# Kernel optimization log

Measured on AMD Instinct MI355X. Metric: run time of the kernel, lower is better.

## Reference

```python
import jax, jax.numpy as jnp
import numpy as np

LN_EPS = 1e-5


def entmax15(z):
    # exact 1.5-entmax over last axis (Peters & Martins sorting algorithm)
    z = z / 2.0
    z = z - jnp.max(z, axis=-1, keepdims=True)  # shift-invariant, for stability
    zs = -jnp.sort(-z, axis=-1)                 # descending sort
    k = jnp.arange(1, z.shape[-1] + 1, dtype=z.dtype)
    mean = jnp.cumsum(zs, axis=-1) / k
    meansq = jnp.cumsum(zs * zs, axis=-1) / k
    ss = k * (meansq - jnp.square(mean))
    delta = (1.0 - ss) / k
    tau = mean - jnp.sqrt(jnp.clip(delta, 0.0))
    support = jnp.sum((tau <= zs).astype(jnp.int32), axis=-1, keepdims=True)
    tau_star = jnp.take_along_axis(tau, support - 1, axis=-1)
    return jnp.square(jnp.clip(z - tau_star, 0.0))


def layernorm_noaffine(v):
    m = jnp.mean(v, axis=-1, keepdims=True)
    var = jnp.mean(jnp.square(v - m), axis=-1, keepdims=True)
    return (v - m) / jnp.sqrt(var + LN_EPS)


def cp_mumoe(x, gate, Win, Wout):
    ones = jnp.ones(x.shape[:-1] + (1,), x.dtype)
    xb = jnp.concatenate([x, ones], axis=-1)
    z = jnp.einsum('btd,dr->btr', xb, Win) * gate  # [b,t,R]
    return jnp.einsum('btr,or->bto', z, Wout)      # [b,t,o]


def setup_inputs() -> dict:
    key = jax.random.key(0)
    ks = jax.random.split(key, 8)
    B, T, D, O, D2, E, R = 8, 2048, 1024, 4096, 1024, 16, 512
    s = lambda k, shape, scale: jax.random.normal(k, shape, jnp.float32) * scale
    return {
        'x': s(ks[0], (B, T, D), 1.0),
        'proj': s(ks[1], (D, E), D ** -0.5),
        'C1': s(ks[2], (E, R), E ** -0.5),
        'Win1': s(ks[3], (D + 1, R), D ** -0.5),
        'Wout1': s(ks[4], (O, R), R ** -0.5),
        'C2': s(ks[5], (E, R), E ** -0.5),
        'Win2': s(ks[6], (O + 1, R), O ** -0.5),
        'Wout2': s(ks[7], (D2, R), R ** -0.5),
    }


def reference(x, proj, C1, Win1, Wout1, C2, Win2, Wout2):
    # expert gating: projection -> LN (no affine) -> 1.5-entmax
    a = entmax15(layernorm_noaffine(jnp.einsum('btd,de->bte', x, proj)))  # [b,t,E]
    # layer 1: CP-decomposed expert mixture (bias folded into input mode)
    g1 = jnp.einsum('bte,er->btr', a, C1)
    h = cp_mumoe(x, g1, Win1, Wout1)
    # GELU + layer 2 reusing the same gate coefficients
    h = jax.nn.gelu(h, approximate=False)
    g2 = jnp.einsum('bte,er->btr', a, C2)
    return cp_mumoe(h, g2, Win2, Wout2)
```

## Files before the change

kernel.cpp:

```cpp
#include <hip/hip_runtime.h>
#include <hip/hip_bf16.h>
#include <math.h>
#include <stdint.h>

typedef unsigned short u16;
typedef __attribute__((ext_vector_type(8))) short bf16x8;
typedef __attribute__((ext_vector_type(4))) float f32x4;
typedef __attribute__((address_space(3))) void* as3_void;
typedef const __attribute__((address_space(1))) void* as1_cvoid;

__device__ inline u16 f2bf(float f) {
    union { float f; unsigned u; } v; v.f = f;
    unsigned r = v.u + 0x7FFFu + ((v.u >> 16) & 1u);
    return (u16)(r >> 16);
}
__device__ inline float bf2f(u16 h) {
    unsigned u = ((unsigned)h) << 16;
    return __builtin_bit_cast(float, u);
}
__device__ inline float gelu_fast(float v) {
    float t = v * fmaf(0.07135702f, v * v, 1.5957691f);
    return v / (1.f + __expf(-t));
}

template<int CTRL, int RM>
__device__ inline float dpp_mov(float v) {
    return __builtin_bit_cast(float, __builtin_amdgcn_update_dpp(
        0, __builtin_bit_cast(int, v), CTRL, RM, 0xf, false));
}
__device__ inline float wave_sum(float v) {
    v += dpp_mov<0x111, 0xf>(v);
    v += dpp_mov<0x112, 0xf>(v);
    v += dpp_mov<0x114, 0xf>(v);
    v += dpp_mov<0x118, 0xf>(v);
    v += dpp_mov<0x142, 0xa>(v);
    v += dpp_mov<0x143, 0xc>(v);
    return v;
}

__global__ __launch_bounds__(256)
void prep_transpose(const float* __restrict__ src, u16* __restrict__ dst,
                    int Rr, int Dd)
{
    __shared__ float t[32][33];
    int tilesR = Rr >> 5;
    int bi = blockIdx.x / tilesR;
    int bj = blockIdx.x - bi * tilesR;
    int d0 = bi * 32, r0 = bj * 32;
    int tr = threadIdx.x >> 3, c4 = threadIdx.x & 7;
    float4 v = *(const float4*)&src[(size_t)(d0 + tr) * Rr + r0 + c4 * 4];
    t[tr][c4 * 4 + 0] = v.x; t[tr][c4 * 4 + 1] = v.y;
    t[tr][c4 * 4 + 2] = v.z; t[tr][c4 * 4 + 3] = v.w;
    __syncthreads();
    short4 o;
    o.x = (short)f2bf(t[c4 * 4 + 0][tr]);
    o.y = (short)f2bf(t[c4 * 4 + 1][tr]);
    o.z = (short)f2bf(t[c4 * 4 + 2][tr]);
    o.w = (short)f2bf(t[c4 * 4 + 3][tr]);
    *(short4*)&dst[(size_t)(r0 + tr) * Dd + d0 + c4 * 4] = o;
}

__global__ __launch_bounds__(256)
void prep_cast(const float* __restrict__ Win1, const float* __restrict__ Wout1,
               const float* __restrict__ Win2, const float* __restrict__ Wout2,
               u16* __restrict__ w1o, u16* __restrict__ w2o,
               float* __restrict__ b1, float* __restrict__ b2)
{
    int idx = blockIdx.x * 256 + threadIdx.x;
    if (idx < 2097152) w1o[idx] = f2bf(Wout1[idx]);
    if (idx < 524288)  w2o[idx] = f2bf(Wout2[idx]);
    if (idx < 512) {
        b1[idx] = Win1[(size_t)1024 * 512 + idx];
        b2[idx] = Win2[(size_t)4096 * 512 + idx];
    }
}

__global__ __launch_bounds__(256)
void k1_proj(const float* __restrict__ x, const float* __restrict__ proj,
             u16* __restrict__ xb, float* __restrict__ sbuf, int Ntok)
{
    __shared__ float plt[16 * 1024];
    const int tid = threadIdx.x;
    #pragma unroll
    for (int k = 0; k < 64; ++k) {
        int idx = k * 256 + tid;
        int e = idx & 15, d = idx >> 4;
        plt[e * 1024 + (d ^ (e << 2))] = proj[idx];
    }
    __syncthreads();

    const int lane = tid & 63;
    const int wid = tid >> 6;
    const int nwaves = gridDim.x * 4;
    const int ngrp = Ntok >> 1;

    for (int grp = blockIdx.x * 4 + wid; grp < ngrp; grp += nwaves) {
        const int t0 = grp * 2;
        float s[16][2];
        #pragma unroll
        for (int e = 0; e < 16; ++e) { s[e][0] = 0.f; s[e][1] = 0.f; }

        #pragma unroll
        for (int j = 0; j < 4; ++j) {
            const int d0 = (j * 64 + lane) * 4;
            float4 xq[2];
            #pragma unroll
            for (int q = 0; q < 2; ++q) {
                xq[q] = *(const float4*)&x[(size_t)(t0 + q) * 1024 + d0];
                short4 h;
                h.x = (short)f2bf(xq[q].x); h.y = (short)f2bf(xq[q].y);
                h.z = (short)f2bf(xq[q].z); h.w = (short)f2bf(xq[q].w);
                *(short4*)&xb[(size_t)(t0 + q) * 1024 + d0] = h;
            }
            #pragma unroll
            for (int e = 0; e < 16; ++e) {
                float4 p = *(const float4*)&plt[e * 1024 + (d0 ^ (e << 2))];
                #pragma unroll
                for (int q = 0; q < 2; ++q) {
                    s[e][q] = fmaf(xq[q].x, p.x, s[e][q]);
                    s[e][q] = fmaf(xq[q].y, p.y, s[e][q]);
                    s[e][q] = fmaf(xq[q].z, p.z, s[e][q]);
                    s[e][q] = fmaf(xq[q].w, p.w, s[e][q]);
                }
            }
        }
        #pragma unroll
        for (int e = 0; e < 16; ++e) {
            s[e][0] = wave_sum(s[e][0]);
            s[e][1] = wave_sum(s[e][1]);
        }
        if (lane == 63) {
            #pragma unroll
            for (int q = 0; q < 2; ++q)
                #pragma unroll
                for (int c = 0; c < 4; ++c) {
                    float4 o = { s[c * 4 + 0][q], s[c * 4 + 1][q],
                                 s[c * 4 + 2][q], s[c * 4 + 3][q] };
                    *(float4*)&sbuf[(size_t)(t0 + q) * 16 + c * 4] = o;
                }
        }
    }
}

__global__ __launch_bounds__(256)
void k1_entmax(const float* __restrict__ sbuf, float* __restrict__ abuf, int Ntok)
{
    int t = blockIdx.x * 256 + threadIdx.x;
    if (t >= Ntok) return;
    float s[16];
    #pragma unroll
    for (int c = 0; c < 4; ++c) {
        float4 v = *(const float4*)&sbuf[(size_t)t * 16 + c * 4];
        s[c * 4 + 0] = v.x; s[c * 4 + 1] = v.y; s[c * 4 + 2] = v.z; s[c * 4 + 3] = v.w;
    }
    float mean = 0.f;
    #pragma unroll
    for (int e = 0; e < 16; ++e) mean += s[e];
    mean *= 0.0625f;
    float var = 0.f;
    #pragma unroll
    for (int e = 0; e < 16; ++e) { float d = s[e] - mean; var = fmaf(d, d, var); }
    var *= 0.0625f;
    float rstd = rsqrtf(var + 1e-5f);

    float z[16];
    #pragma unroll
    for (int e = 0; e < 16; ++e) z[e] = (s[e] - mean) * rstd * 0.5f;
    float zmax = z[0];
    #pragma unroll
    for (int e = 1; e < 16; ++e) zmax = fmaxf(zmax, z[e]);
    #pragma unroll
    for (int e = 0; e < 16; ++e) z[e] -= zmax;

    float zs[16];
    #pragma unroll
    for (int e = 0; e < 16; ++e) zs[e] = z[e];
    #pragma unroll
    for (int k = 2; k <= 16; k <<= 1) {
        #pragma unroll
        for (int j = k >> 1; j > 0; j >>= 1) {
            #pragma unroll
            for (int i = 0; i < 16; ++i) {
                int l = i ^ j;
                if (l > i) {
                    float a = zs[i], b = zs[l];
                    bool asc = ((i & k) == 0);
                    bool sw = asc ? (a > b) : (a < b);
                    if (sw) { zs[i] = b; zs[l] = a; }
                }
            }
        }
    }
    float csum = 0.f, csq = 0.f, tau_star = -3.4e38f;
    #pragma unroll
    for (int kk = 1; kk <= 16; ++kk) {
        float v = zs[16 - kk];
        csum += v; csq += v * v;
        float kf = (float)kk;
        float mn = csum / kf;
        float ms = csq / kf;
        float ss = kf * (ms - mn * mn);
        float delta = fmaxf((1.f - ss) / kf, 0.f);
        float tau = mn - sqrtf(delta);
        if (tau <= v) tau_star = tau;
    }
    #pragma unroll
    for (int c = 0; c < 4; ++c) {
        float4 o;
        float p0 = fmaxf(z[c * 4 + 0] - tau_star, 0.f);
        float p1 = fmaxf(z[c * 4 + 1] - tau_star, 0.f);
        float p2 = fmaxf(z[c * 4 + 2] - tau_star, 0.f);
        float p3 = fmaxf(z[c * 4 + 3] - tau_star, 0.f);
        o.x = p0 * p0; o.y = p1 * p1; o.z = p2 * p2; o.w = p3 * p3;
        *(float4*)&abuf[(size_t)t * 16 + c * 4] = o;
    }
}

__global__ __launch_bounds__(256)
void gcompute(const float* __restrict__ abuf, const float* __restrict__ C1,
              const float* __restrict__ C2, u16* __restrict__ g1,
              u16* __restrict__ g2, int Ntok)
{
    const int tid = threadIdx.x;
    const int lane = tid & 63;
    const int t = blockIdx.x * 4 + (tid >> 6);
    if (t >= Ntok) return;
    float a[16];
    #pragma unroll
    for (int c = 0; c < 4; ++c) {
        float4 v = *(const float4*)&abuf[(size_t)t * 16 + c * 4];
        a[c * 4 + 0] = v.x; a[c * 4 + 1] = v.y; a[c * 4 + 2] = v.z; a[c * 4 + 3] = v.w;
    }
    #pragma unroll
    for (int c8 = 0; c8 < 8; ++c8) {
        int col = c8 * 64 + lane;
        float t1 = 0.f, t2 = 0.f;
        #pragma unroll
        for (int e = 0; e < 16; ++e) {
            t1 = fmaf(a[e], C1[e * 512 + col], t1);
            t2 = fmaf(a[e], C2[e * 512 + col], t2);
        }
        g1[(size_t)t * 512 + col] = f2bf(t1);
        g2[(size_t)t * 512 + col] = f2bf(t2);
    }
}

template<int MODE>
__global__ __launch_bounds__(256, 4)
void gemm_bt(const u16* __restrict__ A, const u16* __restrict__ Bt,
             const float* __restrict__ bias, const u16* __restrict__ gmat,
             void* __restrict__ Cout, int M, int Nn, int K, int tilesN)
{
    __shared__ __align__(1024) char smem[32768];
    const int tid = threadIdx.x;
    const int lane = tid & 63;
    const int wid = tid >> 6;

    int m_t, n_t;
    {
        int bid = blockIdx.x;
        int Mtiles = gridDim.x / tilesN;
        if ((Mtiles & 7) == 0) {
            int xcd = bid & 7, loc = bid >> 3;
            int lm = loc / tilesN;
            m_t = xcd * (Mtiles >> 3) + lm;
            n_t = loc - lm * tilesN;
        } else {
            m_t = bid / tilesN;
            n_t = bid % tilesN;
        }
    }
    const int m0 = m_t * 128;
    const int n0 = n_t * 128;
    const int wm = (wid >> 1) * 64;
    const int wn = (wid & 1) * 64;

    f32x4 acc[4][4];
    #pragma unroll
    for (int i = 0; i < 4; ++i)
        #pragma unroll
        for (int j = 0; j < 4; ++j) acc[i][j] = (f32x4){0.f, 0.f, 0.f, 0.f};

    const int nsteps = K >> 6;
    for (int ks = 0; ks < nsteps; ++ks) {
        const int k0 = ks << 6;
        #pragma unroll
        for (int i = 0; i < 4; ++i) {
            int q = (wid * 4 + i) * 64 + lane;
            int row = q >> 3;
            int c = (q & 7) ^ (row & 7);
            __builtin_amdgcn_global_load_lds(
                (as1_cvoid)(A + (size_t)(m0 + row) * K + k0 + c * 8),
                (as3_void)&smem[(wid * 4 + i) * 1024], 16, 0, 0);
        }
        #pragma unroll
        for (int i = 0; i < 4; ++i) {
            int q = (wid * 4 + i) * 64 + lane;
            int row = q >> 3;
            int c = (q & 7) ^ (row & 7);
            __builtin_amdgcn_global_load_lds(
                (as1_cvoid)(Bt + (size_t)(n0 + row) * K + k0 + c * 8),
                (as3_void)&smem[16384 + (wid * 4 + i) * 1024], 16, 0, 0);
        }
        __syncthreads();
        #pragma unroll
        for (int kk = 0; kk < 2; ++kk) {
            bf16x8 af[4], bfr[4];
            const int slot = kk * 4 + (lane >> 4);
            #pragma unroll
            for (int i = 0; i < 4; ++i) {
                int row = wm + i * 16 + (lane & 15);
                af[i] = *(const bf16x8*)
                    &smem[row * 128 + ((slot ^ (row & 7)) << 4)];
            }
            #pragma unroll
            for (int j = 0; j < 4; ++j) {
                int row = wn + j * 16 + (lane & 15);
                bfr[j] = *(const bf16x8*)
                    &smem[16384 + row * 128 + ((slot ^ (row & 7)) << 4)];
            }
            #pragma unroll
            for (int i = 0; i < 4; ++i)
                #pragma unroll
                for (int j = 0; j < 4; ++j)
                    acc[i][j] = __builtin_amdgcn_mfma_f32_16x16x32_bf16(
                        af[i], bfr[j], acc[i][j], 0, 0, 0);
        }
        __syncthreads();
    }

    const int cl = lane & 15;
    const int rq = (lane >> 4) * 4;
    #pragma unroll
    for (int i = 0; i < 4; ++i) {
        #pragma unroll
        for (int j = 0; j < 4; ++j) {
            int col = n0 + wn + j * 16 + cl;
            float bv = (MODE == 1) ? bias[col] : 0.f;
            #pragma unroll
            for (int r = 0; r < 4; ++r) {
                int row = m0 + wm + i * 16 + rq + r;
                float v = acc[i][j][r];
                if (MODE == 0) {
                    ((u16*)Cout)[(size_t)row * Nn + col] = f2bf(gelu_fast(v));
                } else if (MODE == 1) {
                    v = (v + bv) * bf2f(gmat[(size_t)row * Nn + col]);
                    ((u16*)Cout)[(size_t)row * Nn + col] = f2bf(v);
                } else {
                    ((float*)Cout)[(size_t)row * Nn + col] = v;
                }
            }
        }
    }
}

extern "C" void kernel_launch(void* const* d_in, const int* in_sizes, int n_in,
                              void* d_out, int out_size, void* d_ws, size_t ws_size,
                              hipStream_t stream)
{
    const float* x     = (const float*)d_in[0];
    const float* proj  = (const float*)d_in[1];
    const float* C1    = (const float*)d_in[2];
    const float* Win1  = (const float*)d_in[3];
    const float* Wout1 = (const float*)d_in[4];
    const float* C2    = (const float*)d_in[5];
    const float* Win2  = (const float*)d_in[6];
    const float* Wout2 = (const float*)d_in[7];

    const int D = 1024, O = 4096, R = 512, D2 = 1024;
    const int Ntok = in_sizes[0] / D;

    char* ws = (char*)d_ws;
    size_t off = 0;
    auto alloc = [&](size_t bytes) -> void* {
        void* p = ws + off;
        off += (bytes + 255) & ~(size_t)255;
        return p;
    };
    u16*   z1  = (u16*)  alloc((size_t)Ntok * R * 2);
    u16*   z2  = (u16*)  alloc((size_t)Ntok * R * 2);
    u16*   w1o = (u16*)  alloc((size_t)O * R * 2);
    u16*   w2t = (u16*)  alloc((size_t)R * O * 2);
    u16*   w2o = (u16*)  alloc((size_t)D2 * R * 2);
    float* b1  = (float*)alloc(R * 4);
    float* b2  = (float*)alloc(R * 4);
    size_t persist_end = off;

    u16*   xb   = (u16*)  alloc((size_t)Ntok * D * 2);
    u16*   w1t  = (u16*)  alloc((size_t)R * D * 2);
    float* sbuf = (float*)alloc((size_t)Ntok * 16 * 4);
    float* abuf = (float*)alloc((size_t)Ntok * 16 * 4);

    size_t hAvail = (ws_size > persist_end) ? (ws_size - persist_end) : 0;
    long long chRows = (long long)(hAvail / ((size_t)O * 2));
    chRows &= ~1023LL;
    int CH = (chRows > Ntok) ? Ntok : (int)chRows;
    if (CH < 1024) CH = 1024;
    u16* hbuf = (u16*)(ws + persist_end);

    u16* g1 = z1;
    u16* g2 = z2;

    prep_transpose<<<(D / 32) * (R / 32), 256, 0, stream>>>(Win1, w1t, R, D);
    prep_transpose<<<(O / 32) * (R / 32), 256, 0, stream>>>(Win2, w2t, R, O);
    prep_cast<<<(O * R + 255) / 256, 256, 0, stream>>>(
        Win1, Wout1, Win2, Wout2, w1o, w2o, b1, b2);

    k1_proj  <<<512, 256, 0, stream>>>(x, proj, xb, sbuf, Ntok);
    k1_entmax<<<(Ntok + 255) / 256, 256, 0, stream>>>(sbuf, abuf, Ntok);
    gcompute <<<(Ntok + 3) / 4, 256, 0, stream>>>(abuf, C1, C2, g1, g2, Ntok);

    gemm_bt<1><<<(Ntok / 128) * (R / 128), 256, 0, stream>>>(
        xb, w1t, b1, g1, z1, Ntok, R, D, R / 128);

    for (int r0 = 0; r0 < Ntok; r0 += CH) {
        int cm = Ntok - r0; if (cm > CH) cm = CH;
        gemm_bt<0><<<(cm / 128) * (O / 128), 256, 0, stream>>>(
            z1 + (size_t)r0 * R, w1o, nullptr, nullptr,
            hbuf, cm, O, R, O / 128);
        gemm_bt<1><<<(cm / 128) * (R / 128), 256, 0, stream>>>(
            hbuf, w2t, b2, g2 + (size_t)r0 * R,
            z2 + (size_t)r0 * R, cm, R, O, R / 128);
    }

    gemm_bt<2><<<(Ntok / 128) * (D2 / 128), 256, 0, stream>>>(
        z2, w2o, nullptr, nullptr, d_out, Ntok, D2, R, D2 / 128);
}
```

Before: 330.4 us.

## Add 256x256-tile 8-wave pipelined GEMM for Wout GEMMs with XCD-aware mapping

Introduces a new GEMM kernel with 256x256 output tiles, 512 threads, double-buffered direct global-to-LDS loads interleaved with MFMA phases, s_setprio hints and an XCD-aware block remap. It replaces the 128x128 kernel for the first-layer output projection (with GELU) and the final output projection. Larger tiles raise arithmetic intensity and the staged loads are meant to overlap memory traffic with compute. In exchange the block count drops, occupancy falls to one block per CU with 128KB LDS, and register pressure rises, which may hurt the smaller final GEMM.

```diff
diff --git a/kernel.cpp b/kernel.cpp
--- a/kernel.cpp
+++ b/kernel.cpp
@@ -37,6 +37,8 @@
     v += dpp_mov<0x143, 0xc>(v);
     return v;
 }
+
+#define MFMA16(a, b, c) __builtin_amdgcn_mfma_f32_16x16x32_bf16(a, b, c, 0, 0, 0)
 
 __global__ __launch_bounds__(256)
 void prep_transpose(const float* __restrict__ src, u16* __restrict__ dst,
@@ -323,8 +325,7 @@
             for (int i = 0; i < 4; ++i)
                 #pragma unroll
                 for (int j = 0; j < 4; ++j)
-                    acc[i][j] = __builtin_amdgcn_mfma_f32_16x16x32_bf16(
-                        af[i], bfr[j], acc[i][j], 0, 0, 0);
+                    acc[i][j] = MFMA16(af[i], bfr[j], acc[i][j]);
         }
         __syncthreads();
     }
@@ -346,6 +347,180 @@
                 } else if (MODE == 1) {
                     v = (v + bv) * bf2f(gmat[(size_t)row * Nn + col]);
                     ((u16*)Cout)[(size_t)row * Nn + col] = f2bf(v);
+                } else {
+                    ((float*)Cout)[(size_t)row * Nn + col] = v;
+                }
+            }
+        }
+    }
+}
+
+template<int MODE>
+__global__ __launch_bounds__(512, 1)
+void gemm256p(const u16* __restrict__ A, const u16* __restrict__ Bt,
+              void* __restrict__ Cout, int M, int Nn, int K, int tilesN)
+{
+    __shared__ __align__(1024) char smem[131072];
+    const int tid = threadIdx.x;
+    const int lane = tid & 63;
+    const int wid = tid >> 6;
+    const int wr = wid >> 2;
+    const int wc = wid & 3;
+
+    int m_t, n_t;
+    {
+        int bid = blockIdx.x;
+        int Mtiles = gridDim.x / tilesN;
+        if ((Mtiles & 7) == 0) {
+            int xcd = bid & 7, loc = bid >> 3;
+            int lm = loc / tilesN;
+            m_t = xcd * (Mtiles >> 3) + lm;
+            n_t = loc - lm * tilesN;
+        } else {
+            m_t = bid / tilesN;
+            n_t = bid % tilesN;
+        }
+    }
+    const int m0 = m_t * 256;
+    const int n0 = n_t * 256;
+
+    f32x4 acc[8][4];
+    #pragma unroll
+    for (int i = 0; i < 8; ++i)
+        #pragma unroll
+        for (int j = 0; j < 4; ++j) acc[i][j] = (f32x4){0.f, 0.f, 0.f, 0.f};
+
+    const u16* gA[2][2];
+    const u16* gB[2][2];
+    #pragma unroll
+    for (int h = 0; h < 2; ++h)
+        #pragma unroll
+        for (int i = 0; i < 2; ++i) {
+            int q = h * 1024 + i * 512 + tid;
+            int row = q >> 3;
+            int c = (q & 7) ^ (row & 7);
+            gA[h][i] = A + (size_t)(m0 + row) * K + c * 8;
+            gB[h][i] = Bt + (size_t)(n0 + row) * K + c * 8;
+        }
+    const int dbase = wid * 1024;
+
+    auto stA = [&](int b, int h, int i) {
+        __builtin_amdgcn_global_load_lds((as1_cvoid)gA[h][i],
+            (as3_void)&smem[b * 32768 + h * 16384 + i * 8192 + dbase], 16, 0, 0);
+        gA[h][i] += 64;
+    };
+    auto stB = [&](int b, int h, int i) {
+        __builtin_amdgcn_global_load_lds((as1_cvoid)gB[h][i],
+            (as3_void)&smem[65536 + b * 32768 + h * 16384 + i * 8192 + dbase], 16, 0, 0);
+        gB[h][i] += 64;
+    };
+
+    const int arow = wr * 128 + (lane & 15);
+    const int brow = wc * 64 + (lane & 15);
+    const int sHi = lane >> 4;
+    auto LDA = [&](int b, int i, int kk) -> bf16x8 {
+        int row = arow + i * 16;
+        return *(const bf16x8*)&smem[b * 32768 + row * 128
+            + ((((kk << 2) | sHi) ^ (row & 7)) << 4)];
+    };
+    auto LDB = [&](int b, int j, int kk) -> bf16x8 {
+        int row = brow + j * 16;
+        return *(const bf16x8*)&smem[65536 + b * 32768 + row * 128
+            + ((((kk << 2) | sHi) ^ (row & 7)) << 4)];
+    };
+
+    const int nt = K >> 6;
+    stA(0, 0, 0); stA(0, 0, 1); stA(0, 1, 0); stA(0, 1, 1);
+    stB(0, 0, 0); stB(0, 0, 1); stB(0, 1, 0); stB(0, 1, 1);
+    asm volatile("s_waitcnt vmcnt(0)" ::: "memory");
+    __builtin_amdgcn_sched_barrier(0);
+    __builtin_amdgcn_s_barrier();
+
+    for (int t = 0; t < nt; ++t) {
+        const int b = t & 1;
+        const bool st = (t + 1) < nt;
+        bf16x8 aR[4], bR[4];
+
+        bR[0] = LDB(b, 0, 0); bR[1] = LDB(b, 1, 0);
+        bR[2] = LDB(b, 2, 0); bR[3] = LDB(b, 3, 0);
+        aR[0] = LDA(b, 0, 0); aR[1] = LDA(b, 1, 0);
+        aR[2] = LDA(b, 2, 0); aR[3] = LDA(b, 3, 0);
+        if (st) { stA(b ^ 1, 0, 0); stA(b ^ 1, 0, 1);
+                  stA(b ^ 1, 1, 0); stA(b ^ 1, 1, 1); }
+        __builtin_amdgcn_s_barrier();
+        asm volatile("s_waitcnt lgkmcnt(0)" ::: "memory");
+        __builtin_amdgcn_sched_barrier(0);
+        __builtin_amdgcn_s_setprio(1);
+        #pragma unroll
+        for (int i = 0; i < 4; ++i)
+            #pragma unroll
+            for (int j = 0; j < 4; ++j)
+                acc[i][j] = MFMA16(aR[i], bR[j], acc[i][j]);
+        __builtin_amdgcn_s_setprio(0);
+        __builtin_amdgcn_s_barrier();
+
+        aR[0] = LDA(b, 4, 0); aR[1] = LDA(b, 5, 0);
+        aR[2] = LDA(b, 6, 0); aR[3] = LDA(b, 7, 0);
+        if (st) { stB(b ^ 1, 0, 0); stB(b ^ 1, 0, 1); }
+        __builtin_amdgcn_s_barrier();
+        asm volatile("s_waitcnt lgkmcnt(0)" ::: "memory");
+        __builtin_amdgcn_sched_barrier(0);
+        __builtin_amdgcn_s_setprio(1);
+        #pragma unroll
+        for (int i = 0; i < 4; ++i)
+            #pragma unroll
+            for (int j = 0; j < 4; ++j)
+                acc[4 + i][j] = MFMA16(aR[i], bR[j], acc[4 + i][j]);
+        __builtin_amdgcn_s_setprio(0);
+        __builtin_amdgcn_s_barrier();
+
+        bR[0] = LDB(b, 0, 1); bR[1] = LDB(b, 1, 1);
+        bR[2] = LDB(b, 2, 1); bR[3] = LDB(b, 3, 1);
+        aR[0] = LDA(b, 0, 1); aR[1] = LDA(b, 1, 1);
+        aR[2] = LDA(b, 2, 1); aR[3] = LDA(b, 3, 1);
+        if (st) { stB(b ^ 1, 1, 0); stB(b ^ 1, 1, 1); }
+        __builtin_amdgcn_s_barrier();
+        asm volatile("s_waitcnt lgkmcnt(0)" ::: "memory");
+        __builtin_amdgcn_sched_barrier(0);
+        __builtin_amdgcn_s_setprio(1);
+        #pragma unroll
+        for (int i = 0; i < 4; ++i)
+            #pragma unroll
+            for (int j = 0; j < 4; ++j)
+                acc[i][j] = MFMA16(aR[i], bR[j], acc[i][j]);
+        __builtin_amdgcn_s_setprio(0);
+        __builtin_amdgcn_s_barrier();
+
+        aR[0] = LDA(b, 4, 1); aR[1] = LDA(b, 5, 1);
+        aR[2] = LDA(b, 6, 1); aR[3] = LDA(b, 7, 1);
+        __builtin_amdgcn_s_barrier();
+        asm volatile("s_waitcnt lgkmcnt(0)" ::: "memory");
+        __builtin_amdgcn_sched_barrier(0);
+        __builtin_amdgcn_s_setprio(1);
+        #pragma unroll
+        for (int i = 0; i < 4; ++i)
+            #pragma unroll
+            for (int j = 0; j < 4; ++j)
+                acc[4 + i][j] = MFMA16(aR[i], bR[j], acc[4 + i][j]);
+        __builtin_amdgcn_s_setprio(0);
+        if (st) asm volatile("s_waitcnt vmcnt(0)" ::: "memory");
+        __builtin_amdgcn_sched_barrier(0);
+        __builtin_amdgcn_s_barrier();
+    }
+
+    const int cl = lane & 15;
+    const int rq = (lane >> 4) * 4;
+    #pragma unroll
+    for (int i = 0; i < 8; ++i) {
+        #pragma unroll
+        for (int j = 0; j < 4; ++j) {
+            int col = n0 + wc * 64 + j * 16 + cl;
+            #pragma unroll
+            for (int r = 0; r < 4; ++r) {
+                int row = m0 + wr * 128 + i * 16 + rq + r;
+                float v = acc[i][j][r];
+                if (MODE == 0) {
+                    ((u16*)Cout)[(size_t)row * Nn + col] = f2bf(gelu_fast(v));
                 } else {
                     ((float*)Cout)[(size_t)row * Nn + col] = v;
                 }
@@ -415,14 +590,13 @@
 
     for (int r0 = 0; r0 < Ntok; r0 += CH) {
         int cm = Ntok - r0; if (cm > CH) cm = CH;
-        gemm_bt<0><<<(cm / 128) * (O / 128), 256, 0, stream>>>(
-            z1 + (size_t)r0 * R, w1o, nullptr, nullptr,
-            hbuf, cm, O, R, O / 128);
+        gemm256p<0><<<(cm / 256) * (O / 256), 512, 0, stream>>>(
+            z1 + (size_t)r0 * R, w1o, hbuf, cm, O, R, O / 256);
         gemm_bt<1><<<(cm / 128) * (R / 128), 256, 0, stream>>>(
             hbuf, w2t, b2, g2 + (size_t)r0 * R,
             z2 + (size_t)r0 * R, cm, R, O, R / 128);
     }
 
-    gemm_bt<2><<<(Ntok / 128) * (D2 / 128), 256, 0, stream>>>(
-        z2, w2o, nullptr, nullptr, d_out, Ntok, D2, R, D2 / 128);
-}
+    gemm256p<2><<<(Ntok / 256) * (D2 / 256), 512, 0, stream>>>(
+        z2, w2o, d_out, Ntok, D2, R, D2 / 256);
+}
```

Measured after the change: 336.8 us. About the same (+2.0%).
